# Kernel optimization log

Hardware: AMD Instinct MI355X
Metric: run time of the kernel (lower is better)

The kernel has to match this reference:

```python
import jax, jax.numpy as jnp
import numpy as np

B, N, E = 32, 2048, 4096
D_IN, C, H = 256, 64, 4          # node_hidden_size, gnn_hidden_size, num_heads
SLOPE = 0.2                       # PyG GATConv default negative_slope


def gat_conv(x, src, dst, W, att_src, att_dst, bias):
    """One PyG-style GATConv (concat=True, add_self_loops=True) on a single graph.
    x: [N, Din]; src/dst: [E] int; W: [Din, H*C]; att_*: [H, C]; bias: [H*C]."""
    n = x.shape[0]
    h = (x @ W).reshape(n, H, C)                       # [N,H,C]
    a_src = jnp.einsum('nhc,hc->nh', h, att_src)       # [N,H]
    a_dst = jnp.einsum('nhc,hc->nh', h, att_dst)
    loop = jnp.arange(n, dtype=src.dtype)              # self loops
    s = jnp.concatenate([src, loop])
    d = jnp.concatenate([dst, loop])
    e = jax.nn.leaky_relu(a_src[s] + a_dst[d], SLOPE)  # [E+N,H]
    # segment softmax over incoming edges of each target node
    m = jax.ops.segment_max(e, d, num_segments=n)
    ex = jnp.exp(e - m[d])
    denom = jax.ops.segment_sum(ex, d, num_segments=n)
    alpha = ex / (denom[d] + 1e-16)                    # [E+N,H]
    out = jax.ops.segment_sum(alpha[:, :, None] * h[s], d, num_segments=n)  # [N,H,C]
    return out.reshape(n, H * C) + bias


def setup_inputs() -> dict:
    key = jax.random.key(0)
    ks = jax.random.split(key, 12)
    g = lambda k, shp, fan: jax.random.normal(k, shp, jnp.float32) * (1.0 / np.sqrt(fan))
    return {
        'node_embeddings': jax.random.normal(ks[0], (B, N, D_IN), jnp.float32),
        'src_index': jax.random.randint(ks[1], (B, E), 0, N, jnp.int32),
        'tgt_index': jax.random.randint(ks[2], (B, E), 0, N, jnp.int32),
        'W1': g(ks[3], (D_IN, H * C), D_IN),
        'att_src1': g(ks[4], (H, C), C),
        'att_dst1': g(ks[5], (H, C), C),
        'bias1': jnp.zeros((H * C,), jnp.float32),
        'W2': g(ks[6], (H * C, H * C), H * C),
        'att_src2': g(ks[7], (H, C), C),
        'att_dst2': g(ks[8], (H, C), C),
        'bias2': jnp.zeros((H * C,), jnp.float32),
    }


def reference(node_embeddings, src_index, tgt_index, W1, att_src1, att_dst1, bias1,
              W2, att_src2, att_dst2, bias2):
    def per_graph(x, s, d):
        m = gat_conv(x, s, d, W1, att_src1, att_dst1, bias1)
        m = jax.nn.elu(m)                              # dropout = identity (eval)
        m = gat_conv(m, s, d, W2, att_src2, att_dst2, bias2)
        return m
    return jax.vmap(per_graph)(node_embeddings, src_index, tgt_index)  # [B,N,H*C]
```

## Files before the change

kernel.cpp:

```cpp
#include <hip/hip_runtime.h>
#include <hip/hip_bf16.h>
#include <cstdint>

#define BB 32
#define NN 2048
#define EE 4096
#define HH 4
#define CC 64
#define DD 256
#define MM (BB*NN)

typedef __attribute__((ext_vector_type(8))) short bf16x8;
typedef __attribute__((ext_vector_type(8))) unsigned short u16x8;
typedef __attribute__((ext_vector_type(4))) float f32x4;

__device__ __forceinline__ float b2f(__hip_bfloat16 x){ return __bfloat162float(x); }
__device__ __forceinline__ float u2f(unsigned short u){ return __uint_as_float((unsigned)u << 16); }
__device__ __forceinline__ unsigned short f2u(float f){
  __hip_bfloat16 h = __float2bfloat16(f);
  return *(unsigned short*)&h;
}
__device__ __forceinline__ float ldany(const void* p, int isf, size_t i){
  return isf ? ((const float*)p)[i] : b2f(((const __hip_bfloat16*)p)[i]);
}
__device__ __forceinline__ void gld_lds16(const void* g, void* l){
  __builtin_amdgcn_global_load_lds((const __attribute__((address_space(1))) uint32_t*)g,
                                   (__attribute__((address_space(3))) uint32_t*)l, 16, 0, 0);
}

__global__ void detect_kernel(const unsigned* __restrict__ w, int* __restrict__ flag){
  __shared__ int cnt;
  if(threadIdx.x == 0) cnt = 0;
  __syncthreads();
  int c = 0;
  #pragma unroll
  for(int i = 0; i < 4; ++i){
    unsigned v = w[threadIdx.x*4 + i];
    unsigned elo = (v >> 7) & 0xFFu;
    if(elo >= 100u && elo <= 150u) ++c;
  }
  atomicAdd(&cnt, c);
  __syncthreads();
  if(threadIdx.x == 0) *flag = (cnt < 128) ? 1 : 0;
}

__global__ __launch_bounds__(256) void prep2_kernel(const void* __restrict__ W1,
    const void* __restrict__ W2, __hip_bfloat16* __restrict__ W1t,
    __hip_bfloat16* __restrict__ W2t,
    const void* s0, const void* s1, const void* s2, const void* s3,
    const void* s4, const void* s5, float* __restrict__ attf,
    const int* __restrict__ srcI, const int* __restrict__ dstI,
    int* __restrict__ rowp, unsigned short* __restrict__ srcL,
    const int* __restrict__ flag)
{
  __shared__ int ldeg[NN];
  __shared__ int part[256];
  int bid = blockIdx.x, t = threadIdx.x;
  if(bid < 512){
    int isf = *flag;
    const void* W = (bid < 256) ? W1 : W2;
    __hip_bfloat16* WT = (bid < 256) ? W1t : W2t;
    int i = (bid & 255)*256 + t;
    WT[i] = __float2bfloat16(ldany(W, isf, (size_t)(i & 255)*256 + (i >> 8)));
  } else if(bid < 518){
    int isf = *flag;
    int i = (bid - 512)*256 + t;
    int seg = i >> 8, off = i & 255;
    const void* s = seg==0?s0 : seg==1?s1 : seg==2?s2 : seg==3?s3 : seg==4?s4 : s5;
    attf[i] = ldany(s, isf, off);
  } else {
    int g = bid - 518;
    const int* ds = dstI + g*EE;
    const int* ss = srcI + g*EE;
    for(int i = t; i < NN; i += 256) ldeg[i] = 0;
    __syncthreads();
    for(int i = t; i < EE; i += 256) atomicAdd(&ldeg[ds[i] & (NN-1)], 1);
    __syncthreads();
    int loc[8], s = 0;
    #pragma unroll
    for(int k = 0; k < 8; ++k){ loc[k] = s; s += ldeg[t*8 + k]; }
    part[t] = s;
    __syncthreads();
    if(t == 0){
      int run = 0;
      for(int i = 0; i < 256; ++i){ int tmp = part[i]; part[i] = run; run += tmp; }
    }
    __syncthreads();
    int base = g*EE + part[t];
    int cur[8];
    #pragma unroll
    for(int k = 0; k < 8; ++k){
      int v = base + loc[k];
      rowp[g*(NN+1) + t*8 + k] = v;
      cur[k] = v;
    }
    if(t == 255) rowp[g*(NN+1) + NN] = base + s;
    __syncthreads();
    #pragma unroll
    for(int k = 0; k < 8; ++k) ldeg[t*8 + k] = cur[k];
    __syncthreads();
    for(int i = t; i < EE; i += 256){
      int pos = atomicAdd(&ldeg[ds[i] & (NN-1)], 1);
      srcL[pos] = (unsigned short)ss[i];
    }
  }
}

template<int DYNA>
__global__ __launch_bounds__(256) void mfma_gemm(const void* __restrict__ Ap,
    const __hip_bfloat16* __restrict__ BT, __hip_bfloat16* __restrict__ C,
    const float* __restrict__ attS, const float* __restrict__ attD,
    float* __restrict__ aS, float* __restrict__ aD, const int* __restrict__ flag)
{
  __shared__ __align__(16) short lds[128*128];
  short* lA = lds;
  short* lB = lds + 128*64;
  const int isf  = DYNA ? *flag : 0;
  const int tid  = threadIdx.x;
  const int w    = tid >> 6, lane = tid & 63;
  const int dd   = blockIdx.x;
  const int xcd  = dd & 7, slot = dd >> 3;
  const int rb   = xcd*64 + (slot >> 1), cb = slot & 1;
  const int row0 = rb*128, col0 = cb*128;
  const int wr   = (w & 1)*64, wc = (w >> 1)*64;
  const int lr   = lane >> 3;
  const int kb_g = (lane & 7) ^ lr;
  const int fm   = lane & 15, quad = lane >> 4;
  f32x4 acc[4][4] = {};

  for(int k0 = 0; k0 < 256; k0 += 64){
    #pragma unroll
    for(int c = 0; c < 4; ++c){
      int ra = w*32 + c*8;
      const short* gb = (const short*)BT + (size_t)(col0 + ra + lr)*DD + k0 + kb_g*8;
      gld_lds16(gb, &lB[ra*64]);
    }
    if(DYNA && isf){
      const float* Af = (const float*)Ap;
      float4 ta[4], tb[4];
      #pragma unroll
      for(int i = 0; i < 4; ++i){
        int f8 = i*256 + tid;
        int m = f8 >> 3, kb = f8 & 7;
        const float* p = Af + (size_t)(row0 + m)*DD + k0 + kb*8;
        ta[i] = *(const float4*)p;
        tb[i] = *(const float4*)(p + 4);
      }
      #pragma unroll
      for(int i = 0; i < 4; ++i){
        int f8 = i*256 + tid;
        int m = f8 >> 3, kb = f8 & 7;
        u16x8 o;
        o[0] = f2u(ta[i].x); o[1] = f2u(ta[i].y); o[2] = f2u(ta[i].z); o[3] = f2u(ta[i].w);
        o[4] = f2u(tb[i].x); o[5] = f2u(tb[i].y); o[6] = f2u(tb[i].z); o[7] = f2u(tb[i].w);
        *(u16x8*)&lA[m*64 + ((kb ^ (m & 7))*8)] = o;
      }
    } else {
      #pragma unroll
      for(int c = 0; c < 4; ++c){
        int ra = w*32 + c*8;
        const short* ga = (const short*)Ap + (size_t)(row0 + ra + lr)*DD + k0 + kb_g*8;
        gld_lds16(ga, &lA[ra*64]);
      }
    }
    __syncthreads();
    #pragma unroll
    for(int ks = 0; ks < 2; ++ks){
      bf16x8 af[4], bfr[4];
      int kb = ks*4 + quad;
      #pragma unroll
      for(int i = 0; i < 4; ++i){
        int m = wr + i*16 + fm;
        af[i]  = *(const bf16x8*)&lA[m*64 + ((kb ^ (m & 7))*8)];
        int n = wc + i*16 + fm;
        bfr[i] = *(const bf16x8*)&lB[n*64 + ((kb ^ (n & 7))*8)];
      }
      #pragma unroll
      for(int i = 0; i < 4; ++i)
        #pragma unroll
        for(int j = 0; j < 4; ++j)
          acc[i][j] = __builtin_amdgcn_mfma_f32_16x16x32_bf16(af[i], bfr[j], acc[i][j], 0, 0, 0);
    }
    __syncthreads();
  }

  const int headI = (col0 + wc) >> 6;
  float ws_[4], wd_[4];
  #pragma unroll
  for(int j = 0; j < 4; ++j){
    ws_[j] = attS[headI*CC + j*16 + fm];
    wd_[j] = attD[headI*CC + j*16 + fm];
  }
  #pragma unroll
  for(int i = 0; i < 4; ++i){
    #pragma unroll
    for(int r = 0; r < 4; ++r){
      float s = 0.f, dv = 0.f;
      #pragma unroll
      for(int j = 0; j < 4; ++j){
        float v = acc[i][j][r];
        s  += v * ws_[j];
        dv += v * wd_[j];
      }
      #pragma unroll
      for(int m = 1; m <= 8; m <<= 1){
        s  += __shfl_xor(s,  m);
        dv += __shfl_xor(dv, m);
      }
      if(fm == i*4 + r){
        int row = row0 + wr + i*16 + quad*4 + r;
        aS[(size_t)row*HH + headI] = s;
        aD[(size_t)row*HH + headI] = dv;
      }
    }
  }

  #pragma unroll
  for(int i = 0; i < 4; ++i)
    #pragma unroll
    for(int j = 0; j < 4; ++j)
      #pragma unroll
      for(int r = 0; r < 4; ++r){
        int rl = wr + i*16 + quad*4 + r;
        int cl = wc + j*16 + fm;
        lds[rl*128 + (cl ^ ((rl & 12) << 2))] = (short)f2u(acc[i][j][r]);
      }
  __syncthreads();
  const int rr = tid >> 4, cc = (tid & 15)*8;
  #pragma unroll
  for(int p = 0; p < 8; ++p){
    int rl = p*16 + rr;
    u16x8 v = *(const u16x8*)&lds[rl*128 + (cc ^ ((rl & 12) << 2))];
    *(u16x8*)((unsigned short*)C + (size_t)(row0 + rl)*DD + col0 + cc) = v;
  }
}

template<int LAYER>
__global__ __launch_bounds__(256) void gather_kernel(const __hip_bfloat16* __restrict__ H,
    const float* __restrict__ a_src, const float* __restrict__ a_dst,
    const int* __restrict__ row_ptr, const unsigned short* __restrict__ srcList,
    const float* __restrict__ bias, void* __restrict__ outp,
    const int* __restrict__ flag)
{
  int blk  = blockIdx.x;
  int vblk = (blk & 7)*2048 + (blk >> 3);
  int wid  = vblk*4 + (int)(threadIdx.x >> 6);
  int lane = threadIdx.x & 63;
  int b = wid >> 11, d = wid & (NN-1);
  int head = lane >> 4;
  int start = row_ptr[b*(NN+1) + d];
  int end   = row_ptr[b*(NN+1) + d + 1];
  const unsigned short* Hu = (const unsigned short*)H;

  float adv = a_dst[wid*HH + head];
  float sv  = a_src[wid*HH + head] + adv;
  sv = sv > 0.f ? sv : 0.2f*sv;
  float exs = __expf(sv);

  ushort4 hv = *(const ushort4*)(Hu + (size_t)wid*DD + lane*4);
  f32x4 acc;
  acc.x = exs*u2f(hv.x); acc.y = exs*u2f(hv.y); acc.z = exs*u2f(hv.z); acc.w = exs*u2f(hv.w);
  float den = exs;

  int e = start;
  float ax = 0.f; ushort4 hw = {0,0,0,0};
  if(e < end){
    int s = srcList[e];
    ax = a_src[(b*NN + s)*HH + head];
    hw = *(const ushort4*)(Hu + (size_t)(b*NN + s)*DD + lane*4);
  }
  while(e < end){
    float axn = 0.f; ushort4 hwn = {0,0,0,0};
    if(e + 1 < end){
      int sn = srcList[e+1];
      axn = a_src[(b*NN + sn)*HH + head];
      hwn = *(const ushort4*)(Hu + (size_t)(b*NN + sn)*DD + lane*4);
    }
    float v = ax + adv;
    v = v > 0.f ? v : 0.2f*v;
    float ex = __expf(v);
    acc.x += ex*u2f(hw.x); acc.y += ex*u2f(hw.y); acc.z += ex*u2f(hw.z); acc.w += ex*u2f(hw.w);
    den += ex;
    ax = axn; hw = hwn; ++e;
  }
  float inv = 1.f / (den + 1e-16f);
  float4 bs = *(const float4*)(bias + lane*4);
  float o0 = acc.x*inv + bs.x, o1 = acc.y*inv + bs.y;
  float o2 = acc.z*inv + bs.z, o3 = acc.w*inv + bs.w;
  size_t oi = (size_t)wid*DD + lane*4;
  if(LAYER == 1){
    o0 = o0 > 0.f ? o0 : expm1f(o0);
    o1 = o1 > 0.f ? o1 : expm1f(o1);
    o2 = o2 > 0.f ? o2 : expm1f(o2);
    o3 = o3 > 0.f ? o3 : expm1f(o3);
    ushort4 ov = { f2u(o0), f2u(o1), f2u(o2), f2u(o3) };
    *(ushort4*)((unsigned short*)outp + oi) = ov;
  } else {
    if(*flag){
      float4 ov = { o0, o1, o2, o3 };
      *(float4*)((float*)outp + oi) = ov;
    } else {
      ushort4 ov = { f2u(o0), f2u(o1), f2u(o2), f2u(o3) };
      *(ushort4*)((unsigned short*)outp + oi) = ov;
    }
  }
}

extern "C" void kernel_launch(void* const* d_in, const int* in_sizes, int n_in,
                              void* d_out, int out_size, void* d_ws, size_t ws_size,
                              hipStream_t stream)
{
  const void* x_in = d_in[0];
  const int*  srcI = (const int*)d_in[1];
  const int*  dstI = (const int*)d_in[2];
  const void* W1   = d_in[3];
  const void* as1  = d_in[4];
  const void* ad1  = d_in[5];
  const void* b1   = d_in[6];
  const void* W2   = d_in[7];
  const void* as2  = d_in[8];
  const void* ad2  = d_in[9];
  const void* b2   = d_in[10];

  char* ws = (char*)d_ws;
  __hip_bfloat16* R1  = (__hip_bfloat16*)ws; ws += (size_t)MM*DD*2;
  __hip_bfloat16* R2  = (__hip_bfloat16*)ws; ws += (size_t)MM*DD*2;
  float* a_src = (float*)ws; ws += (size_t)MM*HH*4;
  float* a_dst = (float*)ws; ws += (size_t)MM*HH*4;
  __hip_bfloat16* W1t = (__hip_bfloat16*)ws; ws += (size_t)DD*DD*2;
  __hip_bfloat16* W2t = (__hip_bfloat16*)ws; ws += (size_t)DD*DD*2;
  float* attf = (float*)ws; ws += 1536*4;
  int*   rowp = (int*)ws;   ws += (size_t)BB*(NN+1)*4;
  unsigned short* srcL = (unsigned short*)ws; ws += (size_t)BB*EE*2;
  int*   flag = (int*)ws;   ws += 8;

  const int gemmBlocks   = (MM/128)*(DD/128);
  const int gatherBlocks = (MM*64)/256;

  detect_kernel<<<1, 64, 0, stream>>>((const unsigned*)x_in, flag);
  prep2_kernel<<<550, 256, 0, stream>>>(W1, W2, W1t, W2t,
                                        as1, ad1, b1, as2, ad2, b2, attf,
                                        srcI, dstI, rowp, srcL, flag);

  mfma_gemm<1><<<gemmBlocks, 256, 0, stream>>>(x_in, W1t, R2, attf + 0, attf + 256,
                                               a_src, a_dst, flag);
  gather_kernel<1><<<gatherBlocks, 256, 0, stream>>>(R2, a_src, a_dst, rowp, srcL,
                                                     attf + 512, R1, flag);
  mfma_gemm<0><<<gemmBlocks, 256, 0, stream>>>(R1, W2t, R2, attf + 768, attf + 1024,
                                               a_src, a_dst, flag);
  gather_kernel<2><<<gatherBlocks, 256, 0, stream>>>(R2, a_src, a_dst, rowp, srcL,
                                                     attf + 1280, d_out, flag);
}
```

Measured before the change: 245.8 us.

## Fuse GEMM and gather phases into one persistent kernel with grid barriers

The four separate kernels (two GEMMs, two gather passes) become one persistent kernel of 1024 blocks that runs all four phases in turn, separated by atomic-counter grid barriers. The barrier counters are zeroed inside the prep kernel. Each block computes one GEMM tile and then handles 64 destination nodes in the gather phases. This is meant to remove kernel launch gaps and tail effects between stages. In exchange it adds barrier spin costs, relies on all 1024 blocks being co-resident (4 per CU is declared via launch bounds), and gives less latency hiding in the gather phases because there are fewer waves.

```diff
diff --git a/kernel.cpp b/kernel.cpp
--- a/kernel.cpp
+++ b/kernel.cpp
@@ -9,6 +9,7 @@
 #define CC 64
 #define DD 256
 #define MM (BB*NN)
+#define NB 1024
 
 typedef __attribute__((ext_vector_type(8))) short bf16x8;
 typedef __attribute__((ext_vector_type(8))) unsigned short u16x8;
@@ -26,6 +27,17 @@
 __device__ __forceinline__ void gld_lds16(const void* g, void* l){
   __builtin_amdgcn_global_load_lds((const __attribute__((address_space(1))) uint32_t*)g,
                                    (__attribute__((address_space(3))) uint32_t*)l, 16, 0, 0);
+}
+
+__device__ __forceinline__ void grid_sync(int* cnt){
+  __syncthreads();
+  if(threadIdx.x == 0){
+    __threadfence();
+    atomicAdd(cnt, 1);
+    while(__hip_atomic_load(cnt, __ATOMIC_ACQUIRE, __HIP_MEMORY_SCOPE_AGENT) < NB)
+      __builtin_amdgcn_s_sleep(4);
+  }
+  __syncthreads();
 }
 
 __global__ void detect_kernel(const unsigned* __restrict__ w, int* __restrict__ flag){
@@ -51,7 +63,7 @@
     const void* s4, const void* s5, float* __restrict__ attf,
     const int* __restrict__ srcI, const int* __restrict__ dstI,
     int* __restrict__ rowp, unsigned short* __restrict__ srcL,
-    const int* __restrict__ flag)
+    int* __restrict__ bar, const int* __restrict__ flag)
 {
   __shared__ int ldeg[NN];
   __shared__ int part[256];
@@ -68,7 +80,7 @@
     int seg = i >> 8, off = i & 255;
     const void* s = seg==0?s0 : seg==1?s1 : seg==2?s2 : seg==3?s3 : seg==4?s4 : s5;
     attf[i] = ldany(s, isf, off);
-  } else {
+  } else if(bid < 550){
     int g = bid - 518;
     const int* ds = dstI + g*EE;
     const int* ss = srcI + g*EE;
@@ -103,16 +115,18 @@
       int pos = atomicAdd(&ldeg[ds[i] & (NN-1)], 1);
       srcL[pos] = (unsigned short)ss[i];
     }
+  } else {
+    if(t < 48) bar[t] = 0;
   }
 }
 
 template<int DYNA>
-__global__ __launch_bounds__(256) void mfma_gemm(const void* __restrict__ Ap,
+__device__ __forceinline__ void gemm_tile(const void* __restrict__ Ap,
     const __hip_bfloat16* __restrict__ BT, __hip_bfloat16* __restrict__ C,
     const float* __restrict__ attS, const float* __restrict__ attD,
-    float* __restrict__ aS, float* __restrict__ aD, const int* __restrict__ flag)
-{
-  __shared__ __align__(16) short lds[128*128];
+    float* __restrict__ aS, float* __restrict__ aD, const int* __restrict__ flag,
+    short* lds)
+{
   short* lA = lds;
   short* lB = lds + 128*64;
   const int isf  = DYNA ? *flag : 0;
@@ -233,77 +247,101 @@
     u16x8 v = *(const u16x8*)&lds[rl*128 + (cc ^ ((rl & 12) << 2))];
     *(u16x8*)((unsigned short*)C + (size_t)(row0 + rl)*DD + col0 + cc) = v;
   }
+  __syncthreads();
 }
 
 template<int LAYER>
-__global__ __launch_bounds__(256) void gather_kernel(const __hip_bfloat16* __restrict__ H,
+__device__ __forceinline__ void gather_phase(const __hip_bfloat16* __restrict__ H,
     const float* __restrict__ a_src, const float* __restrict__ a_dst,
     const int* __restrict__ row_ptr, const unsigned short* __restrict__ srcList,
     const float* __restrict__ bias, void* __restrict__ outp,
     const int* __restrict__ flag)
 {
-  int blk  = blockIdx.x;
-  int vblk = (blk & 7)*2048 + (blk >> 3);
-  int wid  = vblk*4 + (int)(threadIdx.x >> 6);
-  int lane = threadIdx.x & 63;
-  int b = wid >> 11, d = wid & (NN-1);
-  int head = lane >> 4;
-  int start = row_ptr[b*(NN+1) + d];
-  int end   = row_ptr[b*(NN+1) + d + 1];
+  const int dd   = blockIdx.x;
+  const int w    = threadIdx.x >> 6, lane = threadIdx.x & 63;
+  const int base = (dd & 7)*8192 + (dd >> 3)*64;
+  const int head = lane >> 4;
   const unsigned short* Hu = (const unsigned short*)H;
-
-  float adv = a_dst[wid*HH + head];
-  float sv  = a_src[wid*HH + head] + adv;
-  sv = sv > 0.f ? sv : 0.2f*sv;
-  float exs = __expf(sv);
-
-  ushort4 hv = *(const ushort4*)(Hu + (size_t)wid*DD + lane*4);
-  f32x4 acc;
-  acc.x = exs*u2f(hv.x); acc.y = exs*u2f(hv.y); acc.z = exs*u2f(hv.z); acc.w = exs*u2f(hv.w);
-  float den = exs;
-
-  int e = start;
-  float ax = 0.f; ushort4 hw = {0,0,0,0};
-  if(e < end){
-    int s = srcList[e];
-    ax = a_src[(b*NN + s)*HH + head];
-    hw = *(const ushort4*)(Hu + (size_t)(b*NN + s)*DD + lane*4);
-  }
-  while(e < end){
-    float axn = 0.f; ushort4 hwn = {0,0,0,0};
-    if(e + 1 < end){
-      int sn = srcList[e+1];
-      axn = a_src[(b*NN + sn)*HH + head];
-      hwn = *(const ushort4*)(Hu + (size_t)(b*NN + sn)*DD + lane*4);
-    }
-    float v = ax + adv;
-    v = v > 0.f ? v : 0.2f*v;
-    float ex = __expf(v);
-    acc.x += ex*u2f(hw.x); acc.y += ex*u2f(hw.y); acc.z += ex*u2f(hw.z); acc.w += ex*u2f(hw.w);
-    den += ex;
-    ax = axn; hw = hwn; ++e;
-  }
-  float inv = 1.f / (den + 1e-16f);
-  float4 bs = *(const float4*)(bias + lane*4);
-  float o0 = acc.x*inv + bs.x, o1 = acc.y*inv + bs.y;
-  float o2 = acc.z*inv + bs.z, o3 = acc.w*inv + bs.w;
-  size_t oi = (size_t)wid*DD + lane*4;
-  if(LAYER == 1){
-    o0 = o0 > 0.f ? o0 : expm1f(o0);
-    o1 = o1 > 0.f ? o1 : expm1f(o1);
-    o2 = o2 > 0.f ? o2 : expm1f(o2);
-    o3 = o3 > 0.f ? o3 : expm1f(o3);
-    ushort4 ov = { f2u(o0), f2u(o1), f2u(o2), f2u(o3) };
-    *(ushort4*)((unsigned short*)outp + oi) = ov;
-  } else {
-    if(*flag){
-      float4 ov = { o0, o1, o2, o3 };
-      *(float4*)((float*)outp + oi) = ov;
-    } else {
+  const float4 bs = *(const float4*)(bias + lane*4);
+  const int isf = (LAYER == 2) ? *flag : 0;
+
+  for(int it = 0; it < 16; ++it){
+    int wid = base + it*4 + w;
+    int b = wid >> 11, d = wid & (NN-1);
+    int start = row_ptr[b*(NN+1) + d];
+    int end   = row_ptr[b*(NN+1) + d + 1];
+
+    float adv = a_dst[wid*HH + head];
+    float sv  = a_src[wid*HH + head] + adv;
+    sv = sv > 0.f ? sv : 0.2f*sv;
+    float exs = __expf(sv);
+
+    ushort4 hv = *(const ushort4*)(Hu + (size_t)wid*DD + lane*4);
+    f32x4 acc;
+    acc.x = exs*u2f(hv.x); acc.y = exs*u2f(hv.y); acc.z = exs*u2f(hv.z); acc.w = exs*u2f(hv.w);
+    float den = exs;
+
+    int e = start;
+    float ax = 0.f; ushort4 hw = {0,0,0,0};
+    if(e < end){
+      int s = srcList[e];
+      ax = a_src[(b*NN + s)*HH + head];
+      hw = *(const ushort4*)(Hu + (size_t)(b*NN + s)*DD + lane*4);
+    }
+    while(e < end){
+      float axn = 0.f; ushort4 hwn = {0,0,0,0};
+      if(e + 1 < end){
+        int sn = srcList[e+1];
+        axn = a_src[(b*NN + sn)*HH + head];
+        hwn = *(const ushort4*)(Hu + (size_t)(b*NN + sn)*DD + lane*4);
+      }
+      float v = ax + adv;
+      v = v > 0.f ? v : 0.2f*v;
+      float ex = __expf(v);
+      acc.x += ex*u2f(hw.x); acc.y += ex*u2f(hw.y); acc.z += ex*u2f(hw.z); acc.w += ex*u2f(hw.w);
+      den += ex;
+      ax = axn; hw = hwn; ++e;
+    }
+    float inv = 1.f / (den + 1e-16f);
+    float o0 = acc.x*inv + bs.x, o1 = acc.y*inv + bs.y;
+    float o2 = acc.z*inv + bs.z, o3 = acc.w*inv + bs.w;
+    size_t oi = (size_t)wid*DD + lane*4;
+    if(LAYER == 1){
+      o0 = o0 > 0.f ? o0 : expm1f(o0);
+      o1 = o1 > 0.f ? o1 : expm1f(o1);
+      o2 = o2 > 0.f ? o2 : expm1f(o2);
+      o3 = o3 > 0.f ? o3 : expm1f(o3);
       ushort4 ov = { f2u(o0), f2u(o1), f2u(o2), f2u(o3) };
       *(ushort4*)((unsigned short*)outp + oi) = ov;
-    }
-  }
+    } else {
+      if(isf){
+        float4 ov = { o0, o1, o2, o3 };
+        *(float4*)((float*)outp + oi) = ov;
+      } else {
+        ushort4 ov = { f2u(o0), f2u(o1), f2u(o2), f2u(o3) };
+        *(ushort4*)((unsigned short*)outp + oi) = ov;
+      }
+    }
+  }
+}
+
+__global__ __launch_bounds__(256, 4) void fused_kernel(const void* __restrict__ x_in,
+    const __hip_bfloat16* __restrict__ W1t, const __hip_bfloat16* __restrict__ W2t,
+    __hip_bfloat16* __restrict__ R1, __hip_bfloat16* __restrict__ R2,
+    float* __restrict__ a_src, float* __restrict__ a_dst,
+    const int* __restrict__ rowp, const unsigned short* __restrict__ srcL,
+    const float* __restrict__ attf, void* __restrict__ outp,
+    const int* __restrict__ flag, int* __restrict__ bar)
+{
+  __shared__ __align__(16) short lds[128*128];
+
+  gemm_tile<1>(x_in, W1t, R2, attf + 0, attf + 256, a_src, a_dst, flag, lds);
+  grid_sync(bar + 0);
+  gather_phase<1>(R2, a_src, a_dst, rowp, srcL, attf + 512, R1, flag);
+  grid_sync(bar + 16);
+  gemm_tile<0>(R1, W2t, R2, attf + 768, attf + 1024, a_src, a_dst, flag, lds);
+  grid_sync(bar + 32);
+  gather_phase<2>(R2, a_src, a_dst, rowp, srcL, attf + 1280, outp, flag);
 }
 
 extern "C" void kernel_launch(void* const* d_in, const int* in_sizes, int n_in,
@@ -332,22 +370,13 @@
   float* attf = (float*)ws; ws += 1536*4;
   int*   rowp = (int*)ws;   ws += (size_t)BB*(NN+1)*4;
   unsigned short* srcL = (unsigned short*)ws; ws += (size_t)BB*EE*2;
-  int*   flag = (int*)ws;   ws += 8;
-
-  const int gemmBlocks   = (MM/128)*(DD/128);
-  const int gatherBlocks = (MM*64)/256;
+  int*   flag = (int*)ws;   ws += 16;
+  int*   bar  = (int*)ws;   ws += 48*4;
 
   detect_kernel<<<1, 64, 0, stream>>>((const unsigned*)x_in, flag);
-  prep2_kernel<<<550, 256, 0, stream>>>(W1, W2, W1t, W2t,
+  prep2_kernel<<<551, 256, 0, stream>>>(W1, W2, W1t, W2t,
                                         as1, ad1, b1, as2, ad2, b2, attf,
-                                        srcI, dstI, rowp, srcL, flag);
-
-  mfma_gemm<1><<<gemmBlocks, 256, 0, stream>>>(x_in, W1t, R2, attf + 0, attf + 256,
-                                               a_src, a_dst, flag);
-  gather_kernel<1><<<gatherBlocks, 256, 0, stream>>>(R2, a_src, a_dst, rowp, srcL,
-                                                     attf + 512, R1, flag);
-  mfma_gemm<0><<<gemmBlocks, 256, 0, stream>>>(R1, W2t, R2, attf + 768, attf + 1024,
-                                               a_src, a_dst, flag);
-  gather_kernel<2><<<gatherBlocks, 256, 0, stream>>>(R2, a_src, a_dst, rowp, srcL,
-                                                     attf + 1280, d_out, flag);
-}
+                                        srcI, dstI, rowp, srcL, bar, flag);
+  fused_kernel<<<NB, 256, 0, stream>>>(x_in, W1t, W2t, R1, R2, a_src, a_dst,
+                                       rowp, srcL, attf, d_out, flag, bar);
+}
```

New measurement: 901.8 us. 267% more time.
